# Optimization experiments

Hardware: AMD Instinct MI355X
Metric: run time of the kernel (lower is better)

## Reference

```python
import jax, jax.numpy as jnp
import numpy as np

INPUT_SIZE = 5
HIDDEN_SIZE = 10
BATCH = 8192
SEQ_LEN = 512


def setup_inputs() -> dict:
    key = jax.random.key(0)
    ks = jax.random.split(key, 7)
    D, H = INPUT_SIZE, HIDDEN_SIZE
    s_ih = 1.0 / np.sqrt(H)
    x = jax.random.normal(ks[0], (BATCH, SEQ_LEN, D), dtype=jnp.float32)
    # nn.LSTMCell params: weight_ih [4H, D], weight_hh [4H, H], biases [4H]
    W_ih = jax.random.uniform(ks[1], (4 * H, D), jnp.float32, -s_ih, s_ih)
    W_hh = jax.random.uniform(ks[2], (4 * H, H), jnp.float32, -s_ih, s_ih)
    b_ih = jax.random.uniform(ks[3], (4 * H,), jnp.float32, -s_ih, s_ih)
    b_hh = jax.random.uniform(ks[4], (4 * H,), jnp.float32, -s_ih, s_ih)
    # nn.Linear(H, 1)
    W_out = jax.random.uniform(ks[5], (1, H), jnp.float32, -s_ih, s_ih)
    b_out = jax.random.uniform(ks[6], (1,), jnp.float32, -s_ih, s_ih)
    return {"x": x, "W_ih": W_ih, "W_hh": W_hh, "b_ih": b_ih,
            "b_hh": b_hh, "W_out": W_out, "b_out": b_out}


def reference(x, W_ih, W_hh, b_ih, b_hh, W_out, b_out):
    # x: [B, T, D]; per-timestep LSTMCell recurrence, then Linear(H, 1) head.
    B = x.shape[0]
    H = W_hh.shape[1]
    xT = jnp.swapaxes(x, 0, 1)  # [T, B, D]

    def step(carry, xt):
        h, c = carry
        gates = xt @ W_ih.T + b_ih + h @ W_hh.T + b_hh  # [B, 4H]
        i, f, g, o = jnp.split(gates, 4, axis=-1)
        c_new = jax.nn.sigmoid(f) * c + jax.nn.sigmoid(i) * jnp.tanh(g)
        h_new = jax.nn.sigmoid(o) * jnp.tanh(c_new)
        return (h_new, c_new), None

    h0 = jnp.zeros((B, H), dtype=x.dtype)
    c0 = jnp.zeros((B, H), dtype=x.dtype)
    (h_final, _), _ = jax.lax.scan(step, (h0, c0), xT)
    return h_final @ W_out.T + b_out  # [B, 1]
```

## Files before the change

### kernel.cpp

```cpp
#include <hip/hip_runtime.h>


#define BATCH  8192
#define SEQLEN 512
#define INSZ   5
#define HID    10
#define BSTEP  8
#define BV     10

#define L2E  1.442695040888963f
#define L2E2 2.885390081777927f

typedef float     f32x4 __attribute__((ext_vector_type(4)));
typedef _Float16  f16x4 __attribute__((ext_vector_type(4)));
typedef unsigned  u32x2 __attribute__((ext_vector_type(2)));

__device__ __forceinline__ unsigned pkh(float a, float b) {
    return __builtin_bit_cast(unsigned, __builtin_amdgcn_cvt_pkrtz(a, b));
}
__device__ __forceinline__ f16x4 mkab(unsigned lo, unsigned hi) {
    u32x2 t; t.x = lo; t.y = hi;
    return __builtin_bit_cast(f16x4, t);
}
__device__ __forceinline__ f32x4 mfma16(f16x4 a, f16x4 b, f32x4 c) {
    return __builtin_amdgcn_mfma_f32_16x16x16f16(a, b, c, 0, 0, 0);
}

__global__ __launch_bounds__(256, 2) void lstm_mfma(
    const float* __restrict__ x,
    const float* __restrict__ Wih,
    const float* __restrict__ Whh,
    const float* __restrict__ bih,
    const float* __restrict__ bhh,
    const float* __restrict__ Wout,
    const float* __restrict__ bout,
    float* __restrict__ out)
{
    const int lane  = threadIdx.x & 63;
    const int wid   = threadIdx.x >> 6;
    const int gwave = (blockIdx.x * blockDim.x + threadIdx.x) >> 6;
    const int col   = lane & 15;
    const int g     = lane >> 4;
    const int q     = col & 3;
    const int sq    = col >> 2;
    const size_t seq = (size_t)gwave * 4 + sq;

    __shared__ unsigned short hsh[4][48];

    if (lane < 48) hsh[wid][lane] = 0;

    f16x4 Af[3];
#pragma unroll
    for (int p = 0; p < 3; ++p) {
        const int rr = 16 * p + col;
        const int rc = (rr < 40) ? rr : 0;
        const int uu = rc >> 2, gate = rc & 3;
        const int orow = gate * HID + uu;
        const float sg = (gate == 2) ? L2E2 : -L2E;
        f16x4 a;
#pragma unroll
        for (int e = 0; e < 4; ++e) {
            const int jj = 4 * g + e;
            float w;
            if (jj < 5)       w = Wih[orow * INSZ + jj];
            else if (jj == 5) w = bih[orow] + bhh[orow];
            else              w = Whh[orow * HID + (jj - 6)];
            if (rr >= 40) w = 0.0f;
            a[e] = (_Float16)(sg * w);
        }
        Af[p] = a;
    }

    const int base = sq * 10;
    const int u    = 4 * q + g;
    const int widx = (u < HID) ? (base + u) : (40 + (lane & 7));
    volatile unsigned short* wp = &hsh[wid][widx];
    const int raidx = (g == 2) ? base + 2 : (g == 3) ? base + 6 : base;
    const int rbidx = (g == 1) ? base : (g == 2) ? base + 4 : (g == 3) ? base + 8 : base;
    volatile const unsigned* pA = (volatile const unsigned*)&hsh[wid][raidx];
    volatile const unsigned* pB = (volatile const unsigned*)&hsh[wid][rbidx];

    const bool isG0 = (g == 0), isG1 = (g == 1);
    const bool isQ0 = (q == 0), isQ1 = (q == 1), isQ2 = (q == 2);

    const float* xp = x + seq * SEQLEN * INSZ;
    float cs = 0.0f;

    f32x4 bufA[BV], bufB[BV];
    {
        const f32x4* v4 = (const f32x4*)xp;
#pragma unroll
        for (int i = 0; i < BV; ++i) bufA[i] = v4[i];
    }
    asm volatile("s_waitcnt lgkmcnt(0)" ::: "memory");

#define DO_STEP(cx, ss)                                                      \
    {                                                                        \
        const unsigned rA = *pA;                                             \
        const unsigned rB = *pB;                                             \
        const int ixb = (ss) * INSZ;                                         \
        const float xv0 = cx[(ixb + 0) >> 2][(ixb + 0) & 3];                 \
        const float xv1 = cx[(ixb + 1) >> 2][(ixb + 1) & 3];                 \
        const float xv2 = cx[(ixb + 2) >> 2][(ixb + 2) & 3];                 \
        const float xv3 = cx[(ixb + 3) >> 2][(ixb + 3) & 3];                 \
        const float xv4 = cx[(ixb + 4) >> 2][(ixb + 4) & 3];                 \
        const unsigned cA0 = pkh(xv0, xv1);             \
        const unsigned cA1 = pkh(xv4, 1.0f);            \
        const unsigned cB0 = pkh(xv2, xv3);             \
        const unsigned pairA = isG0 ? cA0 : (isG1 ? cA1 : rA);               \
        const unsigned pairB = isG0 ? cB0 : rB;                              \
        const f16x4 B0 = mkab(isQ0 ? pairA : 0u, isQ0 ? pairB : 0u);         \
        const f16x4 B1 = mkab(isQ1 ? pairA : 0u, isQ1 ? pairB : 0u);         \
        const f16x4 B2 = mkab(isQ2 ? pairA : 0u, isQ2 ? pairB : 0u);         \
        f32x4 acc = {0.f, 0.f, 0.f, 0.f};                                    \
        acc = mfma16(Af[0], B0, acc);                                        \
        acc = mfma16(Af[1], B1, acc);                                        \
        acc = mfma16(Af[2], B2, acc);                                        \
        const float A_  = __builtin_amdgcn_exp2f(acc[0]);                    \
        const float E1_ = __builtin_amdgcn_exp2f(acc[1]);                    \
        const float U_  = __builtin_amdgcn_exp2f(acc[2]);                    \
        const float Bo_ = __builtin_amdgcn_exp2f(acc[3]);                    \
        const float t1 = 1.0f + A_;                                          \
        const float t2 = 1.0f + E1_;                                         \
        const float t3 = 1.0f + U_;                                          \
        const float um = fmaf(L2E2, U_, -L2E2);            \
        const float m1 = t1 * t3;                                            \
        const float d1 = t2 * m1;                                            \
        const float r1v = __builtin_amdgcn_rcpf(d1);                         \
        const float num = fmaf(cs, m1, um * t2);                             \
        cs = num * r1v;                                                      \
        const float V = __builtin_amdgcn_exp2f(cs);                          \
        const float t4 = 1.0f + Bo_;                                         \
        const float t5 = 1.0f + V;                                           \
        const float r2v = __builtin_amdgcn_rcpf(t4 * t5);                    \
        const float h = (V - 1.0f) * r2v;                                    \
        *wp = __builtin_bit_cast(unsigned short, (_Float16)h);               \
        asm volatile("s_waitcnt lgkmcnt(0)" ::: "memory");                   \
    }

    for (int it = 0; it < SEQLEN / (2 * BSTEP); ++it) {
        const int tb = it * 2 * BSTEP;
        {
            const f32x4* v4 = (const f32x4*)(xp + (tb + BSTEP) * INSZ);
#pragma unroll
            for (int i = 0; i < BV; ++i) bufB[i] = v4[i];
#pragma unroll
            for (int ss = 0; ss < BSTEP; ++ss) DO_STEP(bufA, ss)
        }
        {
            int nb = tb + 2 * BSTEP;
            if (nb > SEQLEN - BSTEP) nb = SEQLEN - BSTEP;
            const f32x4* v4 = (const f32x4*)(xp + nb * INSZ);
#pragma unroll
            for (int i = 0; i < BV; ++i) bufA[i] = v4[i];
#pragma unroll
            for (int ss = 0; ss < BSTEP; ++ss) DO_STEP(bufB, ss)
        }
    }
#undef DO_STEP

    if (g == 0 && q == 0) {
        float r = bout[0];
#pragma unroll
        for (int uu = 0; uu < HID; ++uu) {
            const float hv = (float)__builtin_bit_cast(_Float16, hsh[wid][base + uu]);
            r = fmaf(Wout[uu], hv, r);
        }
        out[gwave * 4 + sq] = r;
    }
}

extern "C" void kernel_launch(void* const* d_in, const int* in_sizes, int n_in,
                              void* d_out, int out_size, void* d_ws, size_t ws_size,
                              hipStream_t stream) {
    const float* x    = (const float*)d_in[0];
    const float* Wih  = (const float*)d_in[1];
    const float* Whh  = (const float*)d_in[2];
    const float* bih  = (const float*)d_in[3];
    const float* bhh  = (const float*)d_in[4];
    const float* Wout = (const float*)d_in[5];
    const float* bout = (const float*)d_in[6];
    float* out = (float*)d_out;

    const int threads = 256;
    const int blocks  = (BATCH * 16) / threads;
    lstm_mfma<<<blocks, threads, 0, stream>>>(x, Wih, Whh, bih, bhh, Wout, bout, out);
}
```

Measured before the change: 138.7 us.

## Replace LDS hidden-state exchange with DPP quad broadcasts and four independent MFMAs

Each lane now keeps its hidden value in a register and shares it through DPP quad_perm broadcasts, so the per-step LDS write, LDS reads and lgkmcnt wait are gone. The weight matrix is re-laid out so every row-quad holds one unit position, which needs four MFMA tiles per step instead of three. The four MFMAs write separate accumulators that are summed afterwards, so they no longer form a dependent chain. The cost is one extra MFMA and several vector adds per step, in exchange for a shorter recurrence critical path.

```diff
diff --git a/kernel.cpp b/kernel.cpp
--- a/kernel.cpp
+++ b/kernel.cpp
@@ -25,6 +25,12 @@
 __device__ __forceinline__ f32x4 mfma16(f16x4 a, f16x4 b, f32x4 c) {
     return __builtin_amdgcn_mfma_f32_16x16x16f16(a, b, c, 0, 0, 0);
 }
+template<int Q>
+__device__ __forceinline__ float quadbcast(float v) {
+    int r = __builtin_amdgcn_update_dpp(0, __builtin_bit_cast(int, v),
+                                        Q * 0x55, 0xF, 0xF, false);
+    return __builtin_bit_cast(float, r);
+}
 
 __global__ __launch_bounds__(256, 2) void lstm_mfma(
     const float* __restrict__ x,
@@ -47,15 +53,17 @@
 
     __shared__ unsigned short hsh[4][48];
 
-    if (lane < 48) hsh[wid][lane] = 0;
+    const int u = 4 * g + q - 6;
+    const bool uvalid = (u >= 0) && (u < HID);
 
-    f16x4 Af[3];
+    f16x4 Af[4];
 #pragma unroll
-    for (int p = 0; p < 3; ++p) {
-        const int rr = 16 * p + col;
-        const int rc = (rr < 40) ? rr : 0;
-        const int uu = rc >> 2, gate = rc & 3;
-        const int orow = gate * HID + uu;
+    for (int p = 0; p < 4; ++p) {
+        const int ug   = 4 * (col >> 2) + p - 6;
+        const int gate = col & 3;
+        const bool v   = (ug >= 0) && (ug < HID);
+        const int uc   = v ? ug : 0;
+        const int orow = gate * HID + uc;
         const float sg = (gate == 2) ? L2E2 : -L2E;
         f16x4 a;
 #pragma unroll
@@ -65,25 +73,16 @@
             if (jj < 5)       w = Wih[orow * INSZ + jj];
             else if (jj == 5) w = bih[orow] + bhh[orow];
             else              w = Whh[orow * HID + (jj - 6)];
-            if (rr >= 40) w = 0.0f;
-            a[e] = (_Float16)(sg * w);
+            a[e] = (_Float16)(v ? sg * w : 0.0f);
         }
         Af[p] = a;
     }
 
-    const int base = sq * 10;
-    const int u    = 4 * q + g;
-    const int widx = (u < HID) ? (base + u) : (40 + (lane & 7));
-    volatile unsigned short* wp = &hsh[wid][widx];
-    const int raidx = (g == 2) ? base + 2 : (g == 3) ? base + 6 : base;
-    const int rbidx = (g == 1) ? base : (g == 2) ? base + 4 : (g == 3) ? base + 8 : base;
-    volatile const unsigned* pA = (volatile const unsigned*)&hsh[wid][raidx];
-    volatile const unsigned* pB = (volatile const unsigned*)&hsh[wid][rbidx];
-
     const bool isG0 = (g == 0), isG1 = (g == 1);
-    const bool isQ0 = (q == 0), isQ1 = (q == 1), isQ2 = (q == 2);
+    const bool isQ0 = (q == 0), isQ1 = (q == 1), isQ2 = (q == 2), isQ3 = (q == 3);
 
     const float* xp = x + seq * SEQLEN * INSZ;
+    float h  = 0.0f;
     float cs = 0.0f;
 
     f32x4 bufA[BV], bufB[BV];
@@ -92,30 +91,35 @@
 #pragma unroll
         for (int i = 0; i < BV; ++i) bufA[i] = v4[i];
     }
-    asm volatile("s_waitcnt lgkmcnt(0)" ::: "memory");
 
 #define DO_STEP(cx, ss)                                                      \
     {                                                                        \
-        const unsigned rA = *pA;                                             \
-        const unsigned rB = *pB;                                             \
         const int ixb = (ss) * INSZ;                                         \
         const float xv0 = cx[(ixb + 0) >> 2][(ixb + 0) & 3];                 \
         const float xv1 = cx[(ixb + 1) >> 2][(ixb + 1) & 3];                 \
         const float xv2 = cx[(ixb + 2) >> 2][(ixb + 2) & 3];                 \
         const float xv3 = cx[(ixb + 3) >> 2][(ixb + 3) & 3];                 \
         const float xv4 = cx[(ixb + 4) >> 2][(ixb + 4) & 3];                 \
-        const unsigned cA0 = pkh(xv0, xv1);             \
-        const unsigned cA1 = pkh(xv4, 1.0f);            \
-        const unsigned cB0 = pkh(xv2, xv3);             \
-        const unsigned pairA = isG0 ? cA0 : (isG1 ? cA1 : rA);               \
-        const unsigned pairB = isG0 ? cB0 : rB;                              \
+               \
+        const float b0 = quadbcast<0>(h), b1 = quadbcast<1>(h);              \
+        const float b2 = quadbcast<2>(h), b3 = quadbcast<3>(h);              \
+        const unsigned hA = pkh(b0, b1), hB = pkh(b2, b3);                   \
+        const unsigned pairA = isG0 ? pkh(xv0, xv1)                          \
+                             : (isG1 ? pkh(xv4, 1.0f) : hA);                 \
+        const unsigned pairB = isG0 ? pkh(xv2, xv3) : hB;                    \
         const f16x4 B0 = mkab(isQ0 ? pairA : 0u, isQ0 ? pairB : 0u);         \
         const f16x4 B1 = mkab(isQ1 ? pairA : 0u, isQ1 ? pairB : 0u);         \
         const f16x4 B2 = mkab(isQ2 ? pairA : 0u, isQ2 ? pairB : 0u);         \
-        f32x4 acc = {0.f, 0.f, 0.f, 0.f};                                    \
-        acc = mfma16(Af[0], B0, acc);                                        \
-        acc = mfma16(Af[1], B1, acc);                                        \
-        acc = mfma16(Af[2], B2, acc);                                        \
+        const f16x4 B3 = mkab(isQ3 ? pairA : 0u, isQ3 ? pairB : 0u);         \
+        f32x4 ac0 = {0.f, 0.f, 0.f, 0.f};                                    \
+        f32x4 ac1 = {0.f, 0.f, 0.f, 0.f};                                    \
+        f32x4 ac2 = {0.f, 0.f, 0.f, 0.f};                                    \
+        f32x4 ac3 = {0.f, 0.f, 0.f, 0.f};                                    \
+        ac0 = mfma16(Af[0], B0, ac0);                                        \
+        ac1 = mfma16(Af[1], B1, ac1);                                        \
+        ac2 = mfma16(Af[2], B2, ac2);                                        \
+        ac3 = mfma16(Af[3], B3, ac3);                                        \
+        const f32x4 acc = (ac0 + ac1) + (ac2 + ac3);                         \
         const float A_  = __builtin_amdgcn_exp2f(acc[0]);                    \
         const float E1_ = __builtin_amdgcn_exp2f(acc[1]);                    \
         const float U_  = __builtin_amdgcn_exp2f(acc[2]);                    \
@@ -133,9 +137,7 @@
         const float t4 = 1.0f + Bo_;                                         \
         const float t5 = 1.0f + V;                                           \
         const float r2v = __builtin_amdgcn_rcpf(t4 * t5);                    \
-        const float h = (V - 1.0f) * r2v;                                    \
-        *wp = __builtin_bit_cast(unsigned short, (_Float16)h);               \
-        asm volatile("s_waitcnt lgkmcnt(0)" ::: "memory");                   \
+        h = (V - 1.0f) * r2v;                                                \
     }
 
     for (int it = 0; it < SEQLEN / (2 * BSTEP); ++it) {
@@ -159,6 +161,10 @@
     }
 #undef DO_STEP
 
+    const int base = sq * 10;
+    const int widx = uvalid ? (base + u) : (40 + (lane & 7));
+    hsh[wid][widx] = __builtin_bit_cast(unsigned short, (_Float16)h);
+    asm volatile("s_waitcnt lgkmcnt(0)" ::: "memory");
     if (g == 0 && q == 0) {
         float r = bout[0];
 #pragma unroll
```

After: 130.4 us. -5.9%, faster.
